# Kernel optimization log

Measured on AMD Instinct MI355X. Metric: run time of the kernel, lower is better.

Reference implementation:

```python
import jax, jax.numpy as jnp
import numpy as np

B, S, D, H = 1, 4096, 1024, 16
DH = D // H

def setup_inputs() -> dict:
    key = jax.random.key(0)
    ks = jax.random.split(key, 5)
    std = float(np.sqrt(2.0 / (D + D)))
    return {
        "x": jax.random.normal(ks[0], (B, S, D), dtype=jnp.float32),
        "Wq": jax.random.normal(ks[1], (D, D), dtype=jnp.float32) * std,
        "Wk": jax.random.normal(ks[2], (D, D), dtype=jnp.float32) * std,
        "Wv": jax.random.normal(ks[3], (D, D), dtype=jnp.float32) * std,
        "Wo": jax.random.normal(ks[4], (D, D), dtype=jnp.float32) * std,
    }

def reference(x, Wq, Wk, Wv, Wo):
    # projections: input @ W.T, then split heads: b s (h d) -> b h s d
    def split_heads(t):
        b, s, _ = t.shape
        return t.reshape(b, s, H, DH).transpose(0, 2, 1, 3)
    q = split_heads(x @ Wq.T)
    k = split_heads(x @ Wk.T)
    v = split_heads(x @ Wv.T)
    scale = 1.0 / jnp.sqrt(jnp.asarray(DH, dtype=x.dtype))
    scores = jnp.einsum("bhqd,bhkd->bhqk", q, k) * scale  # (b,h,s,s)
    # causal mask: allow k <= q
    causal = jnp.tril(jnp.ones((S, S), dtype=bool))
    scores = jnp.where(causal, scores, jnp.finfo(scores.dtype).min)
    attn = jax.nn.softmax(scores, axis=-1)
    out = jnp.einsum("bhqk,bhkd->bhqd", attn, v)  # (b,h,s,d)
    out = out.transpose(0, 2, 1, 3).reshape(B, S, D)  # b h s d -> b s (h d)
    return out @ Wo.T
```

## Files before the change

kernel.cpp:

```cpp
#include <hip/hip_runtime.h>
#include <math.h>

#define SEQ 4096
#define DM  1024
#define NH  16
#define DH  64
#define NS  4

typedef _Float16 h16;
typedef __attribute__((ext_vector_type(4))) _Float16 h16x4;
typedef __attribute__((ext_vector_type(8))) _Float16 h16x8;
typedef __attribute__((ext_vector_type(4))) float f32x4;

__device__ __forceinline__ void gload_lds16(const h16* g, h16* l) {
    __builtin_amdgcn_global_load_lds(
        (const __attribute__((address_space(1))) void*)g,
        (__attribute__((address_space(3))) void*)l, 16, 0, 0);
}

__global__ __launch_bounds__(256) void cvt_all(const float* __restrict__ x,
                                               const float* __restrict__ wq,
                                               const float* __restrict__ wk,
                                               const float* __restrict__ wv,
                                               const float* __restrict__ wo,
                                               h16* __restrict__ dst) {
    const size_t SD4 = (size_t)SEQ * DM / 4;
    const size_t DD4 = (size_t)DM * DM / 4;
    const size_t i = (size_t)blockIdx.x * 256 + threadIdx.x;
    const float* src;
    size_t off;
    if (i < SD4) { src = x; off = i; }
    else {
        const size_t j = i - SD4;
        const int wsel = (int)(j >> 18);
        off = j & (DD4 - 1);
        src = (wsel == 0) ? wq : (wsel == 1) ? wk : (wsel == 2) ? wv : wo;
    }
    const float4 v = ((const float4*)src)[off];
    h16x4 o = { (h16)v.x, (h16)v.y, (h16)v.z, (h16)v.w };
    ((h16x4*)dst)[i] = o;
}

#define GT 32

__global__ __launch_bounds__(256) void gemm_qkv(const h16* __restrict__ xh,
                                                const h16* __restrict__ Wq,
                                                const h16* __restrict__ Wk,
                                                const h16* __restrict__ Wv,
                                                h16* __restrict__ Qh,
                                                h16* __restrict__ Kh,
                                                h16* __restrict__ Vth,
                                                float scl) {
    __shared__ h16 As[2][128 * GT];
    __shared__ h16 Bs[2][128 * GT];

    const int z    = blockIdx.z;
    const h16* B   = (z == 0) ? Wq : (z == 1) ? Wk : Wv;
    const int t    = threadIdx.x;
    const int lane = t & 63;
    const int w    = t >> 6;
    const int wm   = (w >> 1) * 64;
    const int wn   = (w & 1) * 64;
    const int l15  = lane & 15;
    const int lq   = lane >> 4;
    const int lq8  = lq * 8;
    const int m0   = blockIdx.y * 128;
    const int n0   = blockIdx.x * 128;
    const int K = DM, M = SEQ, N = DM;

    const int srow = w * 16 + (lane >> 2);
    const int scol = (lane & 3) * 8;
    const h16* pa0 = xh + (size_t)(m0 + srow) * K + scol;
    const h16* pa1 = xh + (size_t)(m0 + 64 + srow) * K + scol;
    const h16* pb0 = B  + (size_t)(n0 + srow) * K + scol;
    const h16* pb1 = B  + (size_t)(n0 + 64 + srow) * K + scol;

    f32x4 acc[4][4] = {};

    for (int k0 = 0; k0 < K; k0 += 64) {
        __syncthreads();
        #pragma unroll
        for (int s = 0; s < 2; ++s) {
            const int ko = k0 + s * 32;
            gload_lds16(pa0 + ko, &As[s][w * 512]);
            gload_lds16(pa1 + ko, &As[s][2048 + w * 512]);
            gload_lds16(pb0 + ko, &Bs[s][w * 512]);
            gload_lds16(pb1 + ko, &Bs[s][2048 + w * 512]);
        }
        __syncthreads();

        #pragma unroll
        for (int s = 0; s < 2; ++s) {
            h16x8 af[4], bf[4];
            #pragma unroll
            for (int i = 0; i < 4; ++i)
                af[i] = *(const h16x8*)&As[s][(wm + i * 16 + l15) * GT + lq8];
            #pragma unroll
            for (int j = 0; j < 4; ++j)
                bf[j] = *(const h16x8*)&Bs[s][(wn + j * 16 + l15) * GT + lq8];
            #pragma unroll
            for (int i = 0; i < 4; ++i)
                #pragma unroll
                for (int j = 0; j < 4; ++j)
                    acc[i][j] = __builtin_amdgcn_mfma_f32_16x16x32_f16(af[i], bf[j], acc[i][j], 0, 0, 0);
        }
    }

    const int cr = wm + lq * 4;
    const int cc = wn + l15;
    if (z == 2) {
        #pragma unroll
        for (int i = 0; i < 4; ++i)
            #pragma unroll
            for (int j = 0; j < 4; ++j) {
                const int gm0 = m0 + cr + i * 16;
                const int gn  = n0 + cc + j * 16;
                h16x4 v = { (h16)acc[i][j][0], (h16)acc[i][j][1],
                            (h16)acc[i][j][2], (h16)acc[i][j][3] };
                *(h16x4*)(Vth + (size_t)gn * M + gm0) = v;
            }
    } else {
        h16* Og = (z == 0) ? Qh : Kh;
        const float e = (z == 0) ? scl : 1.0f;
        #pragma unroll
        for (int i = 0; i < 4; ++i)
            #pragma unroll
            for (int j = 0; j < 4; ++j)
                #pragma unroll
                for (int r = 0; r < 4; ++r) {
                    const int gm = m0 + cr + i * 16 + r;
                    const int gn = n0 + cc + j * 16;
                    Og[(size_t)gm * N + gn] = (h16)(acc[i][j][r] * e);
                }
    }
}

__global__ __launch_bounds__(256) void gemm_out(const h16* __restrict__ A,
                                                const h16* __restrict__ B,
                                                float* __restrict__ C) {
    __shared__ h16 As[2][64 * GT];
    __shared__ h16 Bs[2][128 * GT];

    const int t    = threadIdx.x;
    const int lane = t & 63;
    const int w    = t >> 6;
    const int wm   = (w >> 1) * 32;
    const int wn   = (w & 1) * 64;
    const int l15  = lane & 15;
    const int lq   = lane >> 4;
    const int lq8  = lq * 8;
    const int m0   = blockIdx.y * 64;
    const int n0   = blockIdx.x * 128;
    const int K = DM, N = DM;

    const int srow = w * 16 + (lane >> 2);
    const int scol = (lane & 3) * 8;
    const h16* pa0 = A + (size_t)(m0 + srow) * K + scol;
    const h16* pb0 = B + (size_t)(n0 + srow) * K + scol;
    const h16* pb1 = B + (size_t)(n0 + 64 + srow) * K + scol;

    f32x4 acc[2][4] = {};

    for (int k0 = 0; k0 < K; k0 += 64) {
        __syncthreads();
        #pragma unroll
        for (int s = 0; s < 2; ++s) {
            const int ko = k0 + s * 32;
            gload_lds16(pa0 + ko, &As[s][w * 512]);
            gload_lds16(pb0 + ko, &Bs[s][w * 512]);
            gload_lds16(pb1 + ko, &Bs[s][2048 + w * 512]);
        }
        __syncthreads();

        #pragma unroll
        for (int s = 0; s < 2; ++s) {
            h16x8 af[2], bf[4];
            #pragma unroll
            for (int i = 0; i < 2; ++i)
                af[i] = *(const h16x8*)&As[s][(wm + i * 16 + l15) * GT + lq8];
            #pragma unroll
            for (int j = 0; j < 4; ++j)
                bf[j] = *(const h16x8*)&Bs[s][(wn + j * 16 + l15) * GT + lq8];
            #pragma unroll
            for (int i = 0; i < 2; ++i)
                #pragma unroll
                for (int j = 0; j < 4; ++j)
                    acc[i][j] = __builtin_amdgcn_mfma_f32_16x16x32_f16(af[i], bf[j], acc[i][j], 0, 0, 0);
        }
    }

    const int cr = wm + lq * 4;
    const int cc = wn + l15;
    #pragma unroll
    for (int i = 0; i < 2; ++i)
        #pragma unroll
        for (int j = 0; j < 4; ++j)
            #pragma unroll
            for (int r = 0; r < 4; ++r)
                C[(size_t)(m0 + cr + i * 16 + r) * N + n0 + cc + j * 16] = acc[i][j][r];
}

#define AST 80
#define VST 72

__global__ __launch_bounds__(256, 3) void flash_attn_split(
        const h16* __restrict__ Qg, const h16* __restrict__ Kg,
        const h16* __restrict__ Vt, h16* __restrict__ OP,
        float* __restrict__ Mb, float* __restrict__ Lb) {
    __shared__ h16 Ks[64 * AST];
    __shared__ h16 Vs[64 * VST];

    const int jq   = 31 - (int)blockIdx.y;
    const int hh   = blockIdx.x;
    const int sp   = blockIdx.z;
    const int t    = threadIdx.x;
    const int lane = t & 63;
    const int w    = t >> 6;
    const int l15  = lane & 15;
    const int lq   = lane >> 4;
    const int lq8  = lq * 8;
    const int hc   = hh * DH;
    const int q0   = jq * 128;
    const int qa   = w * 16 + l15;
    const int diag1 = 2 * jq;
    const int diag2 = 2 * jq + 1;

    const int ntile = 2 * jq + 2;
    const int chunk = (ntile + NS - 1) / NS;
    const int kts   = sp * chunk;
    const int kte   = (kts + chunk < ntile) ? (kts + chunk) : ntile;

    const int r1 = t >> 3;
    const int r2 = r1 + 32;
    const int c1 = (t & 7) * 8;

    const size_t qrow1 = (size_t)(q0 + qa) * DM + hc;
    const size_t qrow2 = (size_t)(q0 + 64 + qa) * DM + hc;
    h16x8 qf[2][2];
    qf[0][0] = *(const h16x8*)(Qg + qrow1 + lq8);
    qf[0][1] = *(const h16x8*)(Qg + qrow1 + 32 + lq8);
    qf[1][0] = *(const h16x8*)(Qg + qrow2 + lq8);
    qf[1][1] = *(const h16x8*)(Qg + qrow2 + 32 + lq8);

    float m_st[2] = { -1e30f, -1e30f };
    f32x4 lacc[2] = {};
    f32x4 o[2][4] = {};
    const h16x4 one4 = { (h16)1.0f, (h16)1.0f, (h16)1.0f, (h16)1.0f };

    h16x8 kv1, kv2, vv1, vv2;

    if (kts < kte) {
        const int kb0 = kts * 64;
        kv1 = *(const h16x8*)(Kg + (size_t)(kb0 + r1) * DM + hc + c1);
        kv2 = *(const h16x8*)(Kg + (size_t)(kb0 + r2) * DM + hc + c1);
        vv1 = *(const h16x8*)(Vt + (size_t)(hc + r1) * SEQ + kb0 + c1);
        vv2 = *(const h16x8*)(Vt + (size_t)(hc + r2) * SEQ + kb0 + c1);
    }

    for (int kt = kts; kt < kte; ++kt) {
        __syncthreads();
        *(h16x8*)&Ks[r1 * AST + c1] = kv1;
        *(h16x8*)&Ks[r2 * AST + c1] = kv2;
        *(h16x8*)&Vs[r1 * VST + c1] = vv1;
        *(h16x8*)&Vs[r2 * VST + c1] = vv2;
        __syncthreads();
        if (kt + 1 < kte) {
            const int k0n = (kt + 1) * 64;
            kv1 = *(const h16x8*)(Kg + (size_t)(k0n + r1) * DM + hc + c1);
            kv2 = *(const h16x8*)(Kg + (size_t)(k0n + r2) * DM + hc + c1);
            vv1 = *(const h16x8*)(Vt + (size_t)(hc + r1) * SEQ + k0n + c1);
            vv2 = *(const h16x8*)(Vt + (size_t)(hc + r2) * SEQ + k0n + c1);
        }

        f32x4 s[2][4] = {};
        #pragma unroll
        for (int kc = 0; kc < 2; ++kc) {
            h16x8 kf[4];
            #pragma unroll
            for (int jj = 0; jj < 4; ++jj)
                kf[jj] = *(const h16x8*)&Ks[(jj * 16 + l15) * AST + kc * 32 + lq8];
            #pragma unroll
            for (int jj = 0; jj < 4; ++jj)
                s[0][jj] = __builtin_amdgcn_mfma_f32_16x16x32_f16(kf[jj], qf[0][kc], s[0][jj], 0, 0, 0);
            #pragma unroll
            for (int jj = 0; jj < 4; ++jj)
                s[1][jj] = __builtin_amdgcn_mfma_f32_16x16x32_f16(kf[jj], qf[1][kc], s[1][jj], 0, 0, 0);
        }

        if (kt >= diag1) {
            const int rel = (q0 + qa) - kt * 64;
            #pragma unroll
            for (int jj = 0; jj < 4; ++jj)
                #pragma unroll
                for (int r = 0; r < 4; ++r)
                    if ((jj * 16 + lq * 4 + r) > rel) s[0][jj][r] = -1e30f;
        }
        if (kt >= diag2) {
            const int rel = (q0 + 64 + qa) - kt * 64;
            #pragma unroll
            for (int jj = 0; jj < 4; ++jj)
                #pragma unroll
                for (int r = 0; r < 4; ++r)
                    if ((jj * 16 + lq * 4 + r) > rel) s[1][jj][r] = -1e30f;
        }

        h16x4 pk[2][4];
        #pragma unroll
        for (int h = 0; h < 2; ++h) {
            const float a0 = fmaxf(fmaxf(s[h][0][0], s[h][0][1]), fmaxf(s[h][0][2], s[h][0][3]));
            const float a1 = fmaxf(fmaxf(s[h][1][0], s[h][1][1]), fmaxf(s[h][1][2], s[h][1][3]));
            const float a2 = fmaxf(fmaxf(s[h][2][0], s[h][2][1]), fmaxf(s[h][2][2], s[h][2][3]));
            const float a3 = fmaxf(fmaxf(s[h][3][0], s[h][3][1]), fmaxf(s[h][3][2], s[h][3][3]));
            float mx = fmaxf(fmaxf(a0, a1), fmaxf(a2, a3));
            mx = fmaxf(mx, __shfl_xor(mx, 16, 64));
            mx = fmaxf(mx, __shfl_xor(mx, 32, 64));
            if (mx > m_st[h] + 5.0f) {
                const float alpha = exp2f(m_st[h] - mx);
                m_st[h] = mx;
                #pragma unroll
                for (int r = 0; r < 4; ++r) lacc[h][r] *= alpha;
                #pragma unroll
                for (int jj = 0; jj < 4; ++jj)
                    #pragma unroll
                    for (int r = 0; r < 4; ++r)
                        o[h][jj][r] *= alpha;
            }
            #pragma unroll
            for (int jj = 0; jj < 4; ++jj) {
                const float p0 = exp2f(s[h][jj][0] - m_st[h]);
                const float p1 = exp2f(s[h][jj][1] - m_st[h]);
                const float p2 = exp2f(s[h][jj][2] - m_st[h]);
                const float p3 = exp2f(s[h][jj][3] - m_st[h]);
                pk[h][jj] = h16x4{ (h16)p0, (h16)p1, (h16)p2, (h16)p3 };
            }
            #pragma unroll
            for (int jj = 0; jj < 4; ++jj)
                lacc[h] = __builtin_amdgcn_mfma_f32_16x16x16f16(one4, pk[h][jj], lacc[h], 0, 0, 0);
        }

        #pragma unroll
        for (int dd = 0; dd < 4; ++dd)
            #pragma unroll
            for (int jj = 0; jj < 4; ++jj) {
                const h16x4 vf = *(const h16x4*)&Vs[(dd * 16 + l15) * VST + jj * 16 + lq * 4];
                o[0][dd] = __builtin_amdgcn_mfma_f32_16x16x16f16(vf, pk[0][jj], o[0][dd], 0, 0, 0);
                o[1][dd] = __builtin_amdgcn_mfma_f32_16x16x16f16(vf, pk[1][jj], o[1][dd], 0, 0, 0);
            }
    }

    h16* const op = OP + (size_t)sp * SEQ * DM;
    #pragma unroll
    for (int h = 0; h < 2; ++h) {
        const int qg_row = q0 + h * 64 + qa;
        const size_t qg = (size_t)qg_row * DM + hc;
        #pragma unroll
        for (int jj = 0; jj < 4; ++jj) {
            h16x4 ov = { (h16)o[h][jj][0], (h16)o[h][jj][1],
                         (h16)o[h][jj][2], (h16)o[h][jj][3] };
            *(h16x4*)(op + qg + jj * 16 + lq * 4) = ov;
        }
        if (lq == 0) {
            const size_t mi = ((size_t)sp * NH + hh) * SEQ + qg_row;
            Mb[mi] = m_st[h];
            Lb[mi] = lacc[h][0];
        }
    }
}

__global__ __launch_bounds__(256) void combine(const h16* __restrict__ OP,
                                               const float* __restrict__ Mb,
                                               const float* __restrict__ Lb,
                                               h16* __restrict__ AOh) {
    const int i  = blockIdx.x * 256 + threadIdx.x;
    const int q  = i >> 8;
    const int c4 = (i & 255) * 4;
    const int hh = c4 >> 6;

    float ms[NS], ls[NS];
    float mstar = -1e30f;
    #pragma unroll
    for (int s = 0; s < NS; ++s) {
        const size_t mi = ((size_t)s * NH + hh) * SEQ + q;
        ms[s] = Mb[mi];
        ls[s] = Lb[mi];
        mstar = fmaxf(mstar, ms[s]);
    }
    float L = 0.0f;
    float acc[4] = {};
    #pragma unroll
    for (int s = 0; s < NS; ++s) {
        const float ws = exp2f(ms[s] - mstar);
        L += ls[s] * ws;
        const h16x4 ov = *(const h16x4*)(OP + (size_t)s * SEQ * DM + (size_t)q * DM + c4);
        acc[0] += ws * (float)ov[0];
        acc[1] += ws * (float)ov[1];
        acc[2] += ws * (float)ov[2];
        acc[3] += ws * (float)ov[3];
    }
    const float inv = 1.0f / L;
    h16x4 r = { (h16)(acc[0] * inv), (h16)(acc[1] * inv),
                (h16)(acc[2] * inv), (h16)(acc[3] * inv) };
    *(h16x4*)(AOh + (size_t)q * DM + c4) = r;
}

extern "C" void kernel_launch(void* const* d_in, const int* in_sizes, int n_in,
                              void* d_out, int out_size, void* d_ws, size_t ws_size,
                              hipStream_t stream) {
    const float* x  = (const float*)d_in[0];
    const float* Wq = (const float*)d_in[1];
    const float* Wk = (const float*)d_in[2];
    const float* Wv = (const float*)d_in[3];
    const float* Wo = (const float*)d_in[4];
    float* out = (float*)d_out;

    const size_t SD = (size_t)SEQ * DM;
    const size_t DD = (size_t)DM * DM;

    h16* xh  = (h16*)d_ws;
    h16* wqh = xh + SD;
    h16* wkh = wqh + DD;
    h16* wvh = wkh + DD;
    h16* woh = wvh + DD;
    h16* Qh  = woh + DD;
    h16* Kh  = Qh + SD;
    h16* Vth = Kh + SD;
    h16* AOh = Vth + SD;
    h16* OP  = AOh + SD;
    float* Mb = (float*)(OP + (size_t)NS * SD);
    float* Lb = Mb + (size_t)NS * NH * SEQ;

    const dim3 blk(256);

    cvt_all<<<(int)((SD + 4 * DD) / 4 / 256), blk, 0, stream>>>(x, Wq, Wk, Wv, Wo, xh);

    const float SCL = 0.125f * 1.44269504088896340736f;

    gemm_qkv<<<dim3(DM / 128, SEQ / 128, 3), blk, 0, stream>>>(
        xh, wqh, wkh, wvh, Qh, Kh, Vth, SCL);

    flash_attn_split<<<dim3(NH, 32, NS), blk, 0, stream>>>(Qh, Kh, Vth, OP, Mb, Lb);

    combine<<<(int)(SD / 4 / 256), blk, 0, stream>>>(OP, Mb, Lb, AOh);

    gemm_out<<<dim3(DM / 128, SEQ / 64), blk, 0, stream>>>(AOh, woh, out);
}
```

Before: 222.1 us.

## Drop split-K flash attention and combine kernel; normalize output in-kernel

Removes the four-way split of the key range across blocks and the separate combine kernel that merged partial outputs using stored max and sum values. Each block now processes its full causal key range and writes the normalized fp16 output directly. This eliminates partial-output writes and reads plus one kernel launch. In exchange the grid shrinks from 2048 to 512 blocks with very uneven per-block work, which can leave compute units idle and lengthen the tail.

Result: slower. 240.3 us (+8.2%).

```diff
diff --git a/kernel.cpp b/kernel.cpp
--- a/kernel.cpp
+++ b/kernel.cpp
@@ -5,7 +5,6 @@
 #define DM  1024
 #define NH  16
 #define DH  64
-#define NS  4
 
 typedef _Float16 h16;
 typedef __attribute__((ext_vector_type(4))) _Float16 h16x4;
@@ -203,16 +202,14 @@
 #define AST 80
 #define VST 72
 
-__global__ __launch_bounds__(256, 3) void flash_attn_split(
+__global__ __launch_bounds__(256, 3) void flash_attn(
         const h16* __restrict__ Qg, const h16* __restrict__ Kg,
-        const h16* __restrict__ Vt, h16* __restrict__ OP,
-        float* __restrict__ Mb, float* __restrict__ Lb) {
+        const h16* __restrict__ Vt, h16* __restrict__ AOh) {
     __shared__ h16 Ks[64 * AST];
     __shared__ h16 Vs[64 * VST];
 
     const int jq   = 31 - (int)blockIdx.y;
     const int hh   = blockIdx.x;
-    const int sp   = blockIdx.z;
     const int t    = threadIdx.x;
     const int lane = t & 63;
     const int w    = t >> 6;
@@ -225,10 +222,7 @@
     const int diag1 = 2 * jq;
     const int diag2 = 2 * jq + 1;
 
-    const int ntile = 2 * jq + 2;
-    const int chunk = (ntile + NS - 1) / NS;
-    const int kts   = sp * chunk;
-    const int kte   = (kts + chunk < ntile) ? (kts + chunk) : ntile;
+    const int kte  = 2 * jq + 2;
 
     const int r1 = t >> 3;
     const int r2 = r1 + 32;
@@ -249,15 +243,12 @@
 
     h16x8 kv1, kv2, vv1, vv2;
 
-    if (kts < kte) {
-        const int kb0 = kts * 64;
-        kv1 = *(const h16x8*)(Kg + (size_t)(kb0 + r1) * DM + hc + c1);
-        kv2 = *(const h16x8*)(Kg + (size_t)(kb0 + r2) * DM + hc + c1);
-        vv1 = *(const h16x8*)(Vt + (size_t)(hc + r1) * SEQ + kb0 + c1);
-        vv2 = *(const h16x8*)(Vt + (size_t)(hc + r2) * SEQ + kb0 + c1);
-    }
-
-    for (int kt = kts; kt < kte; ++kt) {
+    kv1 = *(const h16x8*)(Kg + (size_t)r1 * DM + hc + c1);
+    kv2 = *(const h16x8*)(Kg + (size_t)r2 * DM + hc + c1);
+    vv1 = *(const h16x8*)(Vt + (size_t)(hc + r1) * SEQ + c1);
+    vv2 = *(const h16x8*)(Vt + (size_t)(hc + r2) * SEQ + c1);
+
+    for (int kt = 0; kt < kte; ++kt) {
         __syncthreads();
         *(h16x8*)&Ks[r1 * AST + c1] = kv1;
         *(h16x8*)&Ks[r2 * AST + c1] = kv2;
@@ -348,59 +339,17 @@
             }
     }
 
-    h16* const op = OP + (size_t)sp * SEQ * DM;
     #pragma unroll
     for (int h = 0; h < 2; ++h) {
-        const int qg_row = q0 + h * 64 + qa;
-        const size_t qg = (size_t)qg_row * DM + hc;
+        const float inv = 1.0f / lacc[h][0];
+        const size_t qg = (size_t)(q0 + h * 64 + qa) * DM + hc;
         #pragma unroll
         for (int jj = 0; jj < 4; ++jj) {
-            h16x4 ov = { (h16)o[h][jj][0], (h16)o[h][jj][1],
-                         (h16)o[h][jj][2], (h16)o[h][jj][3] };
-            *(h16x4*)(op + qg + jj * 16 + lq * 4) = ov;
-        }
-        if (lq == 0) {
-            const size_t mi = ((size_t)sp * NH + hh) * SEQ + qg_row;
-            Mb[mi] = m_st[h];
-            Lb[mi] = lacc[h][0];
-        }
-    }
-}
-
-__global__ __launch_bounds__(256) void combine(const h16* __restrict__ OP,
-                                               const float* __restrict__ Mb,
-                                               const float* __restrict__ Lb,
-                                               h16* __restrict__ AOh) {
-    const int i  = blockIdx.x * 256 + threadIdx.x;
-    const int q  = i >> 8;
-    const int c4 = (i & 255) * 4;
-    const int hh = c4 >> 6;
-
-    float ms[NS], ls[NS];
-    float mstar = -1e30f;
-    #pragma unroll
-    for (int s = 0; s < NS; ++s) {
-        const size_t mi = ((size_t)s * NH + hh) * SEQ + q;
-        ms[s] = Mb[mi];
-        ls[s] = Lb[mi];
-        mstar = fmaxf(mstar, ms[s]);
-    }
-    float L = 0.0f;
-    float acc[4] = {};
-    #pragma unroll
-    for (int s = 0; s < NS; ++s) {
-        const float ws = exp2f(ms[s] - mstar);
-        L += ls[s] * ws;
-        const h16x4 ov = *(const h16x4*)(OP + (size_t)s * SEQ * DM + (size_t)q * DM + c4);
-        acc[0] += ws * (float)ov[0];
-        acc[1] += ws * (float)ov[1];
-        acc[2] += ws * (float)ov[2];
-        acc[3] += ws * (float)ov[3];
-    }
-    const float inv = 1.0f / L;
-    h16x4 r = { (h16)(acc[0] * inv), (h16)(acc[1] * inv),
-                (h16)(acc[2] * inv), (h16)(acc[3] * inv) };
-    *(h16x4*)(AOh + (size_t)q * DM + c4) = r;
+            h16x4 ov = { (h16)(o[h][jj][0] * inv), (h16)(o[h][jj][1] * inv),
+                         (h16)(o[h][jj][2] * inv), (h16)(o[h][jj][3] * inv) };
+            *(h16x4*)(AOh + qg + jj * 16 + lq * 4) = ov;
+        }
+    }
 }
 
 extern "C" void kernel_launch(void* const* d_in, const int* in_sizes, int n_in,
@@ -425,9 +374,6 @@
     h16* Kh  = Qh + SD;
     h16* Vth = Kh + SD;
     h16* AOh = Vth + SD;
-    h16* OP  = AOh + SD;
-    float* Mb = (float*)(OP + (size_t)NS * SD);
-    float* Lb = Mb + (size_t)NS * NH * SEQ;
 
     const dim3 blk(256);
 
@@ -438,9 +384,7 @@
     gemm_qkv<<<dim3(DM / 128, SEQ / 128, 3), blk, 0, stream>>>(
         xh, wqh, wkh, wvh, Qh, Kh, Vth, SCL);
 
-    flash_attn_split<<<dim3(NH, 32, NS), blk, 0, stream>>>(Qh, Kh, Vth, OP, Mb, Lb);
-
-    combine<<<(int)(SD / 4 / 256), blk, 0, stream>>>(OP, Mb, Lb, AOh);
+    flash_attn<<<dim3(NH, 32), blk, 0, stream>>>(Qh, Kh, Vth, AOh);
 
     gemm_out<<<dim3(DM / 128, SEQ / 64), blk, 0, stream>>>(AOh, woh, out);
 }
```
